# Kernel tuning notes

Measured on AMD Instinct MI355X. Metric: run time of the kernel, lower is better.

Reference implementation:

```python
import jax, jax.numpy as jnp
import numpy as np

# ---- config mirroring DetectionPostProcessV1 init + quant params ----
B, H, W, A, C = 8, 128, 128, 8, 8      # batch, feature HxW, anchors/cell, num_classes
STRIDE = 8
IMG_W, IMG_H = 1024, 1024               # image_size
INPUT_SHIFT = 4                          # kInputShift -> in_scale = 1/16
EXP_SHIFT = 4                            # from _gen_exp_table with in_scale 1/16
BOX_THR_INT = 9                          # ceil(0.55 * 2**INPUT_SHIFT)
NMS_THR = 128.0 / 256.0                  # ceil(0.5 * 2**kNmsThresholdShift) / 2**8
NMS_MARGIN = 0.0                         # nms_margin (quantized: ceil(0*16)/16)
PRE_K, POST_K = 1024, 300                # pre-NMS candidates, post_nms_top_k
CLASS_OFFSETS = jnp.zeros((C,), jnp.int32)
CLASS_SEP = 4096.0                       # coordinate offset for class-aware NMS


def setup_inputs() -> dict:
    key = jax.random.key(0)
    k1, _ = jax.random.split(key)
    # int8 repr of quantized head outputs (stored as int32 for jax indexing)
    data = jax.random.randint(k1, (B, A * (4 + C), H, W), -128, 128, dtype=jnp.int32)
    # grid anchors: 8 sizes per cell, stride-8 feature map
    sizes = np.array([16, 24, 32, 48, 64, 96, 128, 192], np.float32)
    ys = (np.arange(H, dtype=np.float32) + 0.5) * STRIDE
    xs = (np.arange(W, dtype=np.float32) + 0.5) * STRIDE
    cy, cx = np.meshgrid(ys, xs, indexing="ij")
    cx, cy = cx[..., None], cy[..., None]              # [H,W,1]
    w = np.broadcast_to(sizes, (H, W, A))
    h = np.broadcast_to(sizes, (H, W, A))
    anchors = np.stack([cx - w / 2, cy - h / 2, cx + w / 2, cy + h / 2], -1)
    anchors = jnp.asarray(anchors.reshape(-1, 4).astype(np.float32))  # [N,4] matches [H,W,A] flatten order
    # integer exp table, exactly as _gen_exp_table
    in_scale = 1.0 / (1 << INPUT_SHIFT)
    idx = np.arange(-128, 128, dtype=np.float32) * in_scale
    ev = np.exp(idx)
    exp_table = jnp.asarray(np.round(ev * (1 << EXP_SHIFT)).astype(np.int32))
    return {"data": data, "anchors": anchors, "exp_table": exp_table}


def _post_process(data, anchors, exp_table):
    N = H * W * A
    # [B, A*(4+C), H, W] -> [B, N, 4+C]
    x = data.reshape(B, A, 4 + C, H, W).transpose(0, 3, 4, 1, 2).reshape(B, N, 4 + C)
    box_d = x[..., :4]
    scores_i = x[..., 4:] + CLASS_OFFSETS                      # int scores with class offsets
    # decode: dx,dy via fixed-point shift; dw,dh via int exp table lookup
    dxy = box_d[..., :2].astype(jnp.float32) / (1 << INPUT_SHIFT)
    expv = exp_table[box_d[..., 2:4] + 128].astype(jnp.float32) / (1 << EXP_SHIFT)
    ctr = (anchors[:, :2] + anchors[:, 2:]) * 0.5              # [N,2]
    wh = anchors[:, 2:] - anchors[:, :2]
    pc = ctr + dxy * wh                                        # [B,N,2]
    pwh = wh * expv
    boxes = jnp.concatenate([pc - pwh * 0.5, pc + pwh * 0.5], -1)
    boxes = jnp.clip(boxes, 0.0, jnp.array([IMG_W, IMG_H, IMG_W, IMG_H], jnp.float32))
    # score filter
    best = scores_i.max(-1)
    label = scores_i.argmax(-1).astype(jnp.int32)
    valid = best >= BOX_THR_INT
    score = best.astype(jnp.float32) / (1 << INPUT_SHIFT)
    sc_masked = jnp.where(valid, score, -1e9)
    topv, topi = jax.lax.top_k(sc_masked, PRE_K)               # [B,PRE_K]
    bk = jnp.take_along_axis(boxes, topi[..., None], 1)        # [B,PRE_K,4]
    lk = jnp.take_along_axis(label, topi, 1)
    vk = topv > -1e8
    # class-aware NMS via coordinate offset trick
    ob = bk + lk[..., None].astype(jnp.float32) * CLASS_SEP
    area = (ob[..., 2] - ob[..., 0]) * (ob[..., 3] - ob[..., 1])
    lt = jnp.maximum(ob[:, :, None, :2], ob[:, None, :, :2])
    rb = jnp.minimum(ob[:, :, None, 2:], ob[:, None, :, 2:])
    whi = jnp.clip(rb - lt, 0.0)
    inter = whi[..., 0] * whi[..., 1]
    iou = inter / (area[:, :, None] + area[:, None, :] - inter + 1e-9)  # [B,PRE_K,PRE_K]
    idxr = jnp.arange(PRE_K)

    def body(i, sup):
        alive_i = ~jnp.take(sup, i, axis=1)                    # [B]
        iou_i = jnp.take(iou, i, axis=1)                       # [B,PRE_K]
        s_i = jnp.take(topv, i, axis=1)[:, None]
        cond = (alive_i[:, None] & (iou_i > NMS_THR)
                & (topv <= s_i - NMS_MARGIN) & (idxr > i)[None, :])
        return sup | cond

    sup = jax.lax.fori_loop(0, PRE_K, body, ~vk)
    keep = vk & ~sup
    fs = jnp.where(keep, topv, -1e9)
    outv, outi = jax.lax.top_k(fs, POST_K)
    boxes_out = jnp.take_along_axis(bk, outi[..., None], 1)
    labels = jnp.take_along_axis(lk, outi, 1)
    ok = outv > -1e8
    boxes_out = jnp.where(ok[..., None], boxes_out, 0.0)       # [B,POST_K,4]
    scores_out = jnp.where(ok, outv, 0.0)                      # [B,POST_K]
    labels_out = jnp.where(ok, labels, -1)                     # [B,POST_K]
    return boxes_out, scores_out, labels_out


def reference(data, anchors, exp_table):
    return _post_process(data, anchors, exp_table)
```

## Files before the change

### kernel.cpp

```cpp
#include <hip/hip_runtime.h>
#include <stdint.h>

#define Bb 8
#define PREK 1024
#define POSTK 300
#define NBIN 120
#define NCHUNK 512

__device__ __forceinline__ float clampb(float v){ return fminf(fmaxf(v, 0.0f), 1024.0f); }

__global__ void __launch_bounds__(256) k1_scores(const int* __restrict__ data,
                                                 unsigned short* __restrict__ sc16,
                                                 int* __restrict__ chist){
    int blk = blockIdx.x;
    int b = blk >> 7, h = blk & 127;
    int tid = threadIdx.x;
    int a = tid >> 5, wg = tid & 31;
    int w = wg << 2;
    const int* p = data + (((size_t)(b*96 + a*12 + 4)) << 14) + (h << 7) + w;
    int4 m = *(const int4*)p;
    int4 lb = make_int4(0,0,0,0);
#pragma unroll
    for (int c = 1; c < 8; ++c){
        int4 v = *(const int4*)(p + ((size_t)c << 14));
        if (v.x > m.x){ m.x = v.x; lb.x = c; }
        if (v.y > m.y){ m.y = v.y; lb.y = c; }
        if (v.z > m.z){ m.z = v.z; lb.z = c; }
        if (v.w > m.w){ m.w = v.w; lb.w = c; }
    }
    ushort4 st;
    st.x = (unsigned short)(((m.x + 128) << 8) | lb.x);
    st.y = (unsigned short)(((m.y + 128) << 8) | lb.y);
    st.z = (unsigned short)(((m.z + 128) << 8) | lb.z);
    st.w = (unsigned short)(((m.w + 128) << 8) | lb.w);
    *(ushort4*)(sc16 + (((size_t)(b*8 + a)) << 14) + (h << 7) + w) = st;

    __shared__ int hist[4][NBIN];
    for (int i = tid; i < 4*NBIN; i += 256) ((int*)hist)[i] = 0;
    __syncthreads();
    int q = wg >> 3;
    if (m.x >= 9) atomicAdd(&hist[q][m.x-9], 1);
    if (m.y >= 9) atomicAdd(&hist[q][m.y-9], 1);
    if (m.z >= 9) atomicAdd(&hist[q][m.z-9], 1);
    if (m.w >= 9) atomicAdd(&hist[q][m.w-9], 1);
    __syncthreads();
    int* cb = chist + ((size_t)(b*NCHUNK + h*4)) * NBIN;
    for (int i = tid; i < 4*NBIN; i += 256) cb[i] = ((int*)hist)[i];
}

__global__ void __launch_bounds__(256) k2_select(int* __restrict__ chist, int* __restrict__ gt,
                                                 int* __restrict__ Tb_, int* __restrict__ dmeta){
    int b = blockIdx.x, tid = threadIdx.x;
    __shared__ int hs2[2][NBIN];
    __shared__ int suf[128];
    __shared__ int Tsh;
    __shared__ int sb[512];
    if (tid == 0) Tsh = -1;
    int half = tid >> 7, bin = tid & 127;
    const int* cb = chist + (size_t)b * NCHUNK * NBIN;
    if (bin < NBIN){
        int s = 0;
        const int* p2 = cb + (size_t)half*256*NBIN + bin;
#pragma unroll 8
        for (int ch = 0; ch < 256; ++ch) s += p2[(size_t)ch * NBIN];
        hs2[half][bin] = s;
    }
    __syncthreads();
    int hbin = 0;
    if (tid < 128){
        hbin = (tid < NBIN) ? hs2[0][tid] + hs2[1][tid] : 0;
        suf[tid] = hbin;
    }
    __syncthreads();
    for (int off = 1; off < 128; off <<= 1){
        int v = 0;
        if (tid < 128 && tid + off < 128) v = suf[tid + off];
        __syncthreads();
        if (tid < 128) suf[tid] += v;
        __syncthreads();
    }
    if (tid < NBIN){
        gt[b*128 + tid] = suf[tid] - hbin;
        if (suf[tid] >= PREK) atomicMax(&Tsh, tid);
    }
    __syncthreads();
    int T = Tsh > 0 ? Tsh : 0;
    if (tid == 0) Tb_[b] = T;
    for (int k = tid; k < PREK; k += 256) dmeta[b*PREK + k] = -1;
    int i0 = tid, i1 = tid + 256;
    for (int abin = T; abin < NBIN; ++abin){
        int* basep = chist + (size_t)(b*NCHUNK) * NBIN + abin;
        int v0 = basep[(size_t)i0 * NBIN], v1 = basep[(size_t)i1 * NBIN];
        sb[i0] = v0; sb[i1] = v1;
        __syncthreads();
        for (int off = 1; off < 512; off <<= 1){
            int a0 = (i0 >= off) ? sb[i0 - off] : 0;
            int a1 = (i1 >= off) ? sb[i1 - off] : 0;
            __syncthreads();
            sb[i0] += a0; sb[i1] += a1;
            __syncthreads();
        }
        basep[(size_t)i0 * NBIN] = sb[i0] - v0;
        basep[(size_t)i1 * NBIN] = sb[i1] - v1;
        __syncthreads();
    }
}

__global__ void __launch_bounds__(256) k3_rank(const unsigned short* __restrict__ sc16,
                                               const int* __restrict__ chist,
                                               const int* __restrict__ gt, const int* __restrict__ Tb_,
                                               const int* __restrict__ data,
                                               const float* __restrict__ anchors,
                                               const int* __restrict__ etab,
                                               float4* __restrict__ dbox, int* __restrict__ dmeta){
    int blk = blockIdx.x;
    int b = blk >> 9, ci = blk & 511;
    int tid = threadIdx.x;
    int h = ci >> 2, w0 = (ci & 3) << 5;
    __shared__ unsigned short sc[256];
    __shared__ int wcnt[4][NBIN];
    if (tid < 64){
        int a = tid & 7, wq = tid >> 3;
        ushort4 v4 = *(const ushort4*)(sc16 + (((size_t)(b*8 + a)) << 14) + (h << 7) + w0 + (wq << 2));
        sc[(wq*4 + 0)*8 + a] = v4.x;
        sc[(wq*4 + 1)*8 + a] = v4.y;
        sc[(wq*4 + 2)*8 + a] = v4.z;
        sc[(wq*4 + 3)*8 + a] = v4.w;
    }
    for (int i = tid; i < 4*NBIN; i += 256) ((int*)wcnt)[i] = 0;
    int T = Tb_[b];
    __syncthreads();
    unsigned short v = sc[tid];
    int s = (int)(v >> 8) - 128;
    int bin = s - 9;
    bool qual = (bin >= T);
    int wv = tid >> 6, lane = tid & 63;
    if (qual) atomicAdd(&wcnt[wv][bin], 1);
    __syncthreads();
    int myeq = 0;
    {
        unsigned long long low = (1ull << lane) - 1ull;
        for (int vb = T; vb < NBIN; ++vb){
            unsigned long long bal = __ballot(qual && bin == vb);
            if (!bal) continue;
            if (qual && bin == vb) myeq = __popcll(bal & low);
        }
    }
    if (!qual) return;
    int cross = 0;
    for (int w2 = 0; w2 < wv; ++w2) cross += wcnt[w2][bin];
    int rank = gt[b*128 + bin] + chist[((size_t)(b*NCHUNK) + ci)*NBIN + bin] + cross + myeq;
    if (rank < PREK){
        int n = ci*256 + tid;
        int a = n & 7, wc = (n >> 3) & 127;
        const int* p = data + (((size_t)(b*96 + a*12)) << 14) + (h << 7) + wc;
        int d0 = p[0], d1 = p[1 << 14], d2 = p[2 << 14], d3 = p[3 << 14];
        float4 an = ((const float4*)anchors)[n];
        float cx = __fmul_rn(__fadd_rn(an.x, an.z), 0.5f);
        float cy = __fmul_rn(__fadd_rn(an.y, an.w), 0.5f);
        float wx = __fsub_rn(an.z, an.x), wy = __fsub_rn(an.w, an.y);
        float dx = __fmul_rn((float)d0, 0.0625f), dy = __fmul_rn((float)d1, 0.0625f);
        float ex = __fmul_rn((float)etab[d2 + 128], 0.0625f);
        float ey = __fmul_rn((float)etab[d3 + 128], 0.0625f);
        float pcx = __fadd_rn(cx, __fmul_rn(dx, wx));
        float pcy = __fadd_rn(cy, __fmul_rn(dy, wy));
        float hx = __fmul_rn(__fmul_rn(wx, ex), 0.5f);
        float hy = __fmul_rn(__fmul_rn(wy, ey), 0.5f);
        float x1 = clampb(__fsub_rn(pcx, hx)), y1 = clampb(__fsub_rn(pcy, hy));
        float x2 = clampb(__fadd_rn(pcx, hx)), y2 = clampb(__fadd_rn(pcy, hy));
        dbox[b*PREK + rank] = make_float4(x1, y1, x2, y2);
        dmeta[b*PREK + rank] = (int)v;
    }
}

__global__ void __launch_bounds__(512, 2) k45_nms_out(const float4* __restrict__ dbox,
                                                      const int* __restrict__ dmeta,
                                                      float* __restrict__ out){
    int b = blockIdx.x, tid = threadIdx.x, lane = tid & 63, wv = tid >> 6;
    __shared__ float X1[1024], Y1[1024], X2[1024], Y2[1024], AR[1024];
    __shared__ unsigned char KEEP[1024];
    __shared__ int wq[8][8], wq2[8][8];
    __shared__ int cbs[8], ccn[8];
    __shared__ int wcn[8];
    __shared__ int pbase;

    int v0 = dmeta[b*PREK + tid];
    int v1 = dmeta[b*PREK + 512 + tid];
    float4 bb0 = dbox[b*PREK + tid];
    float4 bb1 = dbox[b*PREK + 512 + tid];
    bool valid0 = (v0 >= 0), valid1 = (v1 >= 0);
    int lc0 = valid0 ? (v0 & 255) : -1;
    int lc1 = valid1 ? (v1 & 255) : -1;
    KEEP[tid] = 0; KEEP[tid + 512] = 0;
    if (tid == 0) pbase = 0;
    int win0 = 0, win1 = 0;
#pragma unroll
    for (int c = 0; c < 8; ++c){
        unsigned long long bal0 = __ballot(lc0 == c);
        unsigned long long bal1 = __ballot(lc1 == c);
        if (lane == 0){ wq[wv][c] = __popcll(bal0); wq2[wv][c] = __popcll(bal1); }
        if (lc0 == c) win0 = __popcll(bal0 & ((1ull << lane) - 1ull));
        if (lc1 == c) win1 = __popcll(bal1 & ((1ull << lane) - 1ull));
    }
    __syncthreads();
    if (tid < 8){
        int run = 0;
        for (int w2 = 0; w2 < 8; ++w2){ int t = wq[w2][tid];  wq[w2][tid]  = run; run += t; }
        for (int w2 = 0; w2 < 8; ++w2){ int t = wq2[w2][tid]; wq2[w2][tid] = run; run += t; }
        ccn[tid] = run;
    }
    __syncthreads();
    if (tid == 0){
        int run = 0;
        for (int c = 0; c < 8; ++c){ cbs[c] = run; run += ccn[c]; }
    }
    __syncthreads();
    int p0 = 0, p1 = 0;
    if (valid0){
        p0 = cbs[lc0] + wq[wv][lc0] + win0;
        float off = (float)(lc0 << 12);
        float ox1 = __fadd_rn(bb0.x, off), oy1 = __fadd_rn(bb0.y, off);
        float ox2 = __fadd_rn(bb0.z, off), oy2 = __fadd_rn(bb0.w, off);
        X1[p0] = ox1; Y1[p0] = oy1; X2[p0] = ox2; Y2[p0] = oy2;
        AR[p0] = __fmul_rn(__fsub_rn(ox2, ox1), __fsub_rn(oy2, oy1));
    }
    if (valid1){
        p1 = cbs[lc1] + wq2[wv][lc1] + win1;
        float off = (float)(lc1 << 12);
        float ox1 = __fadd_rn(bb1.x, off), oy1 = __fadd_rn(bb1.y, off);
        float ox2 = __fadd_rn(bb1.z, off), oy2 = __fadd_rn(bb1.w, off);
        X1[p1] = ox1; Y1[p1] = oy1; X2[p1] = ox2; Y2[p1] = oy2;
        AR[p1] = __fmul_rn(__fsub_rn(ox2, ox1), __fsub_rn(oy2, oy1));
    }
    __syncthreads();

    {
        int M = ccn[wv], base = cbs[wv];
        if (M > 0 && M <= 256){
            float rx1[4], ry1[4], rx2[4], ry2[4], rar[4];
#pragma unroll
            for (int g = 0; g < 4; ++g){
                int r = g*64 + lane;
                int ad = base + ((r < M) ? r : 0);
                rx1[g]=X1[ad]; ry1[g]=Y1[ad]; rx2[g]=X2[ad]; ry2[g]=Y2[ad]; rar[g]=AR[ad];
            }
            unsigned long long mk[4][4];
#pragma unroll
            for (int g = 0; g < 4; ++g)
#pragma unroll
                for (int w2 = 0; w2 < 4; ++w2) mk[g][w2] = 0ull;

#pragma unroll
            for (int jw = 0; jw < 4; ++jw){
                if (jw*64 < M){
                    int limj = M - jw*64; if (limj > 64) limj = 64;
#pragma unroll 8
                    for (int jl = 0; jl < 64; ++jl){
                        if (jl < limj){
                            int j = jw*64 + jl;
                            float jx1 = __shfl(rx1[jw], jl);
                            float jy1 = __shfl(ry1[jw], jl);
                            float jx2 = __shfl(rx2[jw], jl);
                            float jy2 = __shfl(ry2[jw], jl);
                            float jar = __shfl(rar[jw], jl);
#pragma unroll
                            for (int g = 0; g < 4; ++g){
                                if (g*64 < M){
                                    int i = g*64 + lane;
                                    float wx = fmaxf(__fsub_rn(fminf(rx2[g], jx2), fmaxf(rx1[g], jx1)), 0.0f);
                                    float wy = fmaxf(__fsub_rn(fminf(ry2[g], jy2), fmaxf(ry1[g], jy1)), 0.0f);
                                    float inter = __fmul_rn(wx, wy);
                                    float den = __fadd_rn(__fsub_rn(__fadd_rn(rar[g], jar), inter), 1e-9f);
                                    bool o = (__fdiv_rn(inter, den) > 0.5f) && (j > i);
                                    mk[g][jw] |= o ? (1ull << jl) : 0ull;
                                }
                            }
                        }
                    }
                }
            }

            unsigned long long r0=0ull, r1=0ull, r2=0ull, r3=0ull;
#pragma unroll
            for (int iw = 0; iw < 4; ++iw){
                if (iw*64 < M){
                    int limi = M - iw*64; if (limi > 64) limi = 64;
#pragma unroll 8
                    for (int il = 0; il < 64; ++il){
                        if (il < limi){
                            unsigned long long cur = (iw==0)?r0:(iw==1)?r1:(iw==2)?r2:r3;
                            unsigned long long w0 = __shfl(mk[iw][0], il);
                            unsigned long long w1 = __shfl(mk[iw][1], il);
                            unsigned long long w2_ = __shfl(mk[iw][2], il);
                            unsigned long long w3_ = __shfl(mk[iw][3], il);
                            unsigned long long msk = ((cur >> il) & 1ull) ? 0ull : ~0ull;
                            r0 |= w0 & msk; r1 |= w1 & msk; r2 |= w2_ & msk; r3 |= w3_ & msk;
                        }
                    }
                }
            }
#pragma unroll
            for (int g = 0; g < 4; ++g){
                int r = g*64 + lane;
                unsigned long long rg = (g==0)?r0:(g==1)?r1:(g==2)?r2:r3;
                if (r < M) KEEP[base + r] = (unsigned char)(((rg >> lane) & 1ull) ^ 1ull);
            }
        } else if (M > 256){
            for (int m = lane; m < M; m += 64) KEEP[base+m] = 0;
            for (int i = 0; i < M; ++i){
                if (KEEP[base+i]) continue;
                float xi1 = X1[base+i], yi1 = Y1[base+i];
                float xi2 = X2[base+i], yi2 = Y2[base+i], ai = AR[base+i];
                for (int j = i + 1 + lane; j < M; j += 64){
                    if (KEEP[base+j]) continue;
                    float wx = fmaxf(__fsub_rn(fminf(xi2, X2[base+j]), fmaxf(xi1, X1[base+j])), 0.0f);
                    float wy = fmaxf(__fsub_rn(fminf(yi2, Y2[base+j]), fmaxf(yi1, Y1[base+j])), 0.0f);
                    float inter = __fmul_rn(wx, wy);
                    float den = __fadd_rn(__fsub_rn(__fadd_rn(ai, AR[base+j]), inter), 1e-9f);
                    if (__fdiv_rn(inter, den) > 0.5f) KEEP[base+j] = 1;
                }
            }
            for (int m = lane; m < M; m += 64) KEEP[base+m] ^= 1;
        }
    }
    __syncthreads();

    float* boxes  = out;
    float* scores = out + Bb*POSTK*4;
    float* labs   = out + Bb*POSTK*5;
#pragma unroll
    for (int pass = 0; pass < 2; ++pass){
        bool vld   = pass ? valid1 : valid0;
        int  pp    = pass ? p1 : p0;
        int  lcc   = pass ? lc1 : lc0;
        int  vv    = pass ? v1 : v0;
        float4 bbb = pass ? bb1 : bb0;
        bool kp = vld && (KEEP[pp] != 0);
        unsigned long long bal = __ballot(kp);
        if (lane == 0) wcn[wv] = __popcll(bal);
        __syncthreads();
        if (tid == 0){
            int r = pbase;
            for (int w2 = 0; w2 < 8; ++w2){ int t = wcn[w2]; wcn[w2] = r; r += t; }
            pbase = r;
        }
        __syncthreads();
        int pos = wcn[wv] + __popcll(bal & ((1ull << lane) - 1ull));
        if (kp && pos < POSTK){
            float sval = __fmul_rn((float)((vv >> 8) - 128), 0.0625f);
            int o = (b*POSTK + pos)*4;
            boxes[o+0] = bbb.x; boxes[o+1] = bbb.y; boxes[o+2] = bbb.z; boxes[o+3] = bbb.w;
            scores[b*POSTK + pos] = sval;
            labs[b*POSTK + pos] = (float)lcc;
        }
        __syncthreads();
    }
    int tot = pbase < POSTK ? pbase : POSTK;
    if (tid >= tot && tid < POSTK){
        int o = (b*POSTK + tid)*4;
        boxes[o+0] = 0.f; boxes[o+1] = 0.f; boxes[o+2] = 0.f; boxes[o+3] = 0.f;
        scores[b*POSTK + tid] = 0.f;
        labs[b*POSTK + tid] = -1.0f;
    }
}

extern "C" void kernel_launch(void* const* d_in, const int* in_sizes, int n_in,
                              void* d_out, int out_size, void* d_ws, size_t ws_size,
                              hipStream_t stream) {
    const int*   data    = (const int*)d_in[0];
    const float* anchors = (const float*)d_in[1];
    const int*   etab    = (const int*)d_in[2];
    float* out = (float*)d_out;

    char* ws = (char*)d_ws;
    size_t off = 0;
    auto alloc = [&](size_t bytes)->char*{ char* p = ws + off; off += (bytes + 255) & ~(size_t)255; return p; };
    unsigned short* sc16 = (unsigned short*)alloc((size_t)Bb*8*16384*2);
    int* chist           = (int*)alloc((size_t)Bb*NCHUNK*NBIN*4);
    int* gt              = (int*)alloc((size_t)Bb*128*4);
    int* Tb_             = (int*)alloc((size_t)Bb*4);
    float4* dbox         = (float4*)alloc((size_t)Bb*PREK*16);
    int* dmeta           = (int*)alloc((size_t)Bb*PREK*4);
    (void)ws_size; (void)in_sizes; (void)n_in; (void)out_size;

    k1_scores<<<Bb*128, 256, 0, stream>>>(data, sc16, chist);
    k2_select<<<Bb, 256, 0, stream>>>(chist, gt, Tb_, dmeta);
    k3_rank<<<Bb*NCHUNK, 256, 0, stream>>>(sc16, chist, gt, Tb_, data, anchors, etab, dbox, dmeta);
    k45_nms_out<<<Bb, 512, 0, stream>>>(dbox, dmeta, out);
}
```

Measured before the change: 156.2 us.

## Specialize NMS bitmask path by class size and widen histogram reduction

After: 143.9 us. 7.9% less time.

```diff
diff --git a/kernel.cpp b/kernel.cpp
--- a/kernel.cpp
+++ b/kernel.cpp
@@ -48,27 +48,35 @@
     for (int i = tid; i < 4*NBIN; i += 256) cb[i] = ((int*)hist)[i];
 }
 
-__global__ void __launch_bounds__(256) k2_select(int* __restrict__ chist, int* __restrict__ gt,
-                                                 int* __restrict__ Tb_, int* __restrict__ dmeta){
+__global__ void __launch_bounds__(1024) k2_select(int* __restrict__ chist, int* __restrict__ gt,
+                                                  int* __restrict__ Tb_, int* __restrict__ dmeta){
     int b = blockIdx.x, tid = threadIdx.x;
-    __shared__ int hs2[2][NBIN];
+    __shared__ int part[8][NBIN];
+    __shared__ int hs[NBIN];
     __shared__ int suf[128];
     __shared__ int Tsh;
     __shared__ int sb[512];
     if (tid == 0) Tsh = -1;
-    int half = tid >> 7, bin = tid & 127;
     const int* cb = chist + (size_t)b * NCHUNK * NBIN;
-    if (bin < NBIN){
+    if (tid < 8*NBIN){
+        int g = tid / NBIN, bin = tid - g*NBIN;
         int s = 0;
-        const int* p2 = cb + (size_t)half*256*NBIN + bin;
+        const int* p2 = cb + (size_t)g*64*NBIN + bin;
 #pragma unroll 8
-        for (int ch = 0; ch < 256; ++ch) s += p2[(size_t)ch * NBIN];
-        hs2[half][bin] = s;
+        for (int ch = 0; ch < 64; ++ch) s += p2[(size_t)ch * NBIN];
+        part[g][bin] = s;
+    }
+    __syncthreads();
+    if (tid < NBIN){
+        int s = 0;
+#pragma unroll
+        for (int g = 0; g < 8; ++g) s += part[g][tid];
+        hs[tid] = s;
     }
     __syncthreads();
     int hbin = 0;
     if (tid < 128){
-        hbin = (tid < NBIN) ? hs2[0][tid] + hs2[1][tid] : 0;
+        hbin = (tid < NBIN) ? hs[tid] : 0;
         suf[tid] = hbin;
     }
     __syncthreads();
@@ -86,22 +94,20 @@
     __syncthreads();
     int T = Tsh > 0 ? Tsh : 0;
     if (tid == 0) Tb_[b] = T;
-    for (int k = tid; k < PREK; k += 256) dmeta[b*PREK + k] = -1;
-    int i0 = tid, i1 = tid + 256;
+    dmeta[b*PREK + tid] = -1;
     for (int abin = T; abin < NBIN; ++abin){
         int* basep = chist + (size_t)(b*NCHUNK) * NBIN + abin;
-        int v0 = basep[(size_t)i0 * NBIN], v1 = basep[(size_t)i1 * NBIN];
-        sb[i0] = v0; sb[i1] = v1;
+        int v = 0;
+        if (tid < 512){ v = basep[(size_t)tid * NBIN]; sb[tid] = v; }
         __syncthreads();
         for (int off = 1; off < 512; off <<= 1){
-            int a0 = (i0 >= off) ? sb[i0 - off] : 0;
-            int a1 = (i1 >= off) ? sb[i1 - off] : 0;
+            int a2 = 0;
+            if (tid < 512 && tid >= off) a2 = sb[tid - off];
             __syncthreads();
-            sb[i0] += a0; sb[i1] += a1;
+            if (tid < 512) sb[tid] += a2;
             __syncthreads();
         }
-        basep[(size_t)i0 * NBIN] = sb[i0] - v0;
-        basep[(size_t)i1 * NBIN] = sb[i1] - v1;
+        if (tid < 512) basep[(size_t)tid * NBIN] = sb[tid] - v;
         __syncthreads();
     }
 }
@@ -173,7 +179,81 @@
     }
 }
 
-__global__ void __launch_bounds__(512, 2) k45_nms_out(const float4* __restrict__ dbox,
+template<int NG>
+__device__ __forceinline__ void nms_reg(const float* __restrict__ X1, const float* __restrict__ Y1,
+                                        const float* __restrict__ X2, const float* __restrict__ Y2,
+                                        const float* __restrict__ AR,
+                                        int base, int M, int lane, unsigned char* __restrict__ KEEP){
+    float rx1[NG], ry1[NG], rx2[NG], ry2[NG], rar[NG];
+#pragma unroll
+    for (int g = 0; g < NG; ++g){
+        int r = g*64 + lane;
+        int ad = base + ((r < M) ? r : 0);
+        rx1[g]=X1[ad]; ry1[g]=Y1[ad]; rx2[g]=X2[ad]; ry2[g]=Y2[ad]; rar[g]=AR[ad];
+    }
+    unsigned long long mk[NG][NG];
+#pragma unroll
+    for (int g = 0; g < NG; ++g)
+#pragma unroll
+        for (int c = 0; c < NG; ++c) mk[g][c] = 0ull;
+
+#pragma unroll
+    for (int jw = 0; jw < NG; ++jw){
+        if (jw*64 < M){
+            int limj = M - jw*64; if (limj > 64) limj = 64;
+#pragma unroll 4
+            for (int jl = 0; jl < 64; ++jl){
+                if (jl < limj){
+                    float jx1 = __shfl(rx1[jw], jl);
+                    float jy1 = __shfl(ry1[jw], jl);
+                    float jx2 = __shfl(rx2[jw], jl);
+                    float jy2 = __shfl(ry2[jw], jl);
+                    float jar = __fmul_rn(__fsub_rn(jx2, jx1), __fsub_rn(jy2, jy1));
+#pragma unroll
+                    for (int g = 0; g < NG; ++g){
+                        if (g > jw) continue;
+                        bool jgi = (g < jw) ? true : (lane < jl);
+                        float wx = fmaxf(__fsub_rn(fminf(rx2[g], jx2), fmaxf(rx1[g], jx1)), 0.0f);
+                        float wy = fmaxf(__fsub_rn(fminf(ry2[g], jy2), fmaxf(ry1[g], jy1)), 0.0f);
+                        float inter = __fmul_rn(wx, wy);
+                        float den = __fadd_rn(__fsub_rn(__fadd_rn(rar[g], jar), inter), 1e-9f);
+                        bool o = (__fdiv_rn(inter, den) > 0.5f) && jgi;
+                        mk[g][jw] |= o ? (1ull << jl) : 0ull;
+                    }
+                }
+            }
+        }
+    }
+
+    unsigned long long rem[NG];
+#pragma unroll
+    for (int g = 0; g < NG; ++g) rem[g] = 0ull;
+#pragma unroll
+    for (int iw = 0; iw < NG; ++iw){
+        if (iw*64 < M){
+            int limi = M - iw*64; if (limi > 64) limi = 64;
+#pragma unroll 4
+            for (int il = 0; il < 64; ++il){
+                if (il < limi){
+                    unsigned long long msk = ((rem[iw] >> il) & 1ull) ? 0ull : ~0ull;
+#pragma unroll
+                    for (int w = iw; w < NG; ++w){
+                        unsigned long long rw = __shfl(mk[iw][w], il);
+                        rem[w] |= rw & msk;
+                    }
+                }
+            }
+        }
+    }
+#pragma unroll
+    for (int g = 0; g < NG; ++g){
+        int r = g*64 + lane;
+        unsigned long long rg = rem[g];
+        if (r < M) KEEP[base + r] = (unsigned char)(((rg >> lane) & 1ull) ^ 1ull);
+    }
+}
+
+__global__ void __launch_bounds__(512, 1) k45_nms_out(const float4* __restrict__ dbox,
                                                       const int* __restrict__ dmeta,
                                                       float* __restrict__ out){
     int b = blockIdx.x, tid = threadIdx.x, lane = tid & 63, wv = tid >> 6;
@@ -236,91 +316,27 @@
 
     {
         int M = ccn[wv], base = cbs[wv];
-        if (M > 0 && M <= 256){
-            float rx1[4], ry1[4], rx2[4], ry2[4], rar[4];
-#pragma unroll
-            for (int g = 0; g < 4; ++g){
-                int r = g*64 + lane;
-                int ad = base + ((r < M) ? r : 0);
-                rx1[g]=X1[ad]; ry1[g]=Y1[ad]; rx2[g]=X2[ad]; ry2[g]=Y2[ad]; rar[g]=AR[ad];
-            }
-            unsigned long long mk[4][4];
-#pragma unroll
-            for (int g = 0; g < 4; ++g)
-#pragma unroll
-                for (int w2 = 0; w2 < 4; ++w2) mk[g][w2] = 0ull;
-
-#pragma unroll
-            for (int jw = 0; jw < 4; ++jw){
-                if (jw*64 < M){
-                    int limj = M - jw*64; if (limj > 64) limj = 64;
-#pragma unroll 8
-                    for (int jl = 0; jl < 64; ++jl){
-                        if (jl < limj){
-                            int j = jw*64 + jl;
-                            float jx1 = __shfl(rx1[jw], jl);
-                            float jy1 = __shfl(ry1[jw], jl);
-                            float jx2 = __shfl(rx2[jw], jl);
-                            float jy2 = __shfl(ry2[jw], jl);
-                            float jar = __shfl(rar[jw], jl);
-#pragma unroll
-                            for (int g = 0; g < 4; ++g){
-                                if (g*64 < M){
-                                    int i = g*64 + lane;
-                                    float wx = fmaxf(__fsub_rn(fminf(rx2[g], jx2), fmaxf(rx1[g], jx1)), 0.0f);
-                                    float wy = fmaxf(__fsub_rn(fminf(ry2[g], jy2), fmaxf(ry1[g], jy1)), 0.0f);
-                                    float inter = __fmul_rn(wx, wy);
-                                    float den = __fadd_rn(__fsub_rn(__fadd_rn(rar[g], jar), inter), 1e-9f);
-                                    bool o = (__fdiv_rn(inter, den) > 0.5f) && (j > i);
-                                    mk[g][jw] |= o ? (1ull << jl) : 0ull;
-                                }
-                            }
-                        }
+        if (M > 0){
+            if (M <= 128)      nms_reg<2>(X1, Y1, X2, Y2, AR, base, M, lane, KEEP);
+            else if (M <= 192) nms_reg<3>(X1, Y1, X2, Y2, AR, base, M, lane, KEEP);
+            else if (M <= 256) nms_reg<4>(X1, Y1, X2, Y2, AR, base, M, lane, KEEP);
+            else {
+                for (int m = lane; m < M; m += 64) KEEP[base+m] = 0;
+                for (int i = 0; i < M; ++i){
+                    if (KEEP[base+i]) continue;
+                    float xi1 = X1[base+i], yi1 = Y1[base+i];
+                    float xi2 = X2[base+i], yi2 = Y2[base+i], ai = AR[base+i];
+                    for (int j = i + 1 + lane; j < M; j += 64){
+                        if (KEEP[base+j]) continue;
+                        float wx = fmaxf(__fsub_rn(fminf(xi2, X2[base+j]), fmaxf(xi1, X1[base+j])), 0.0f);
+                        float wy = fmaxf(__fsub_rn(fminf(yi2, Y2[base+j]), fmaxf(yi1, Y1[base+j])), 0.0f);
+                        float inter = __fmul_rn(wx, wy);
+                        float den = __fadd_rn(__fsub_rn(__fadd_rn(ai, AR[base+j]), inter), 1e-9f);
+                        if (__fdiv_rn(inter, den) > 0.5f) KEEP[base+j] = 1;
                     }
                 }
+                for (int m = lane; m < M; m += 64) KEEP[base+m] ^= 1;
             }
-
-            unsigned long long r0=0ull, r1=0ull, r2=0ull, r3=0ull;
-#pragma unroll
-            for (int iw = 0; iw < 4; ++iw){
-                if (iw*64 < M){
-                    int limi = M - iw*64; if (limi > 64) limi = 64;
-#pragma unroll 8
-                    for (int il = 0; il < 64; ++il){
-                        if (il < limi){
-                            unsigned long long cur = (iw==0)?r0:(iw==1)?r1:(iw==2)?r2:r3;
-                            unsigned long long w0 = __shfl(mk[iw][0], il);
-                            unsigned long long w1 = __shfl(mk[iw][1], il);
-                            unsigned long long w2_ = __shfl(mk[iw][2], il);
-                            unsigned long long w3_ = __shfl(mk[iw][3], il);
-                            unsigned long long msk = ((cur >> il) & 1ull) ? 0ull : ~0ull;
-                            r0 |= w0 & msk; r1 |= w1 & msk; r2 |= w2_ & msk; r3 |= w3_ & msk;
-                        }
-                    }
-                }
-            }
-#pragma unroll
-            for (int g = 0; g < 4; ++g){
-                int r = g*64 + lane;
-                unsigned long long rg = (g==0)?r0:(g==1)?r1:(g==2)?r2:r3;
-                if (r < M) KEEP[base + r] = (unsigned char)(((rg >> lane) & 1ull) ^ 1ull);
-            }
-        } else if (M > 256){
-            for (int m = lane; m < M; m += 64) KEEP[base+m] = 0;
-            for (int i = 0; i < M; ++i){
-                if (KEEP[base+i]) continue;
-                float xi1 = X1[base+i], yi1 = Y1[base+i];
-                float xi2 = X2[base+i], yi2 = Y2[base+i], ai = AR[base+i];
-                for (int j = i + 1 + lane; j < M; j += 64){
-                    if (KEEP[base+j]) continue;
-                    float wx = fmaxf(__fsub_rn(fminf(xi2, X2[base+j]), fmaxf(xi1, X1[base+j])), 0.0f);
-                    float wy = fmaxf(__fsub_rn(fminf(yi2, Y2[base+j]), fmaxf(yi1, Y1[base+j])), 0.0f);
-                    float inter = __fmul_rn(wx, wy);
-                    float den = __fadd_rn(__fsub_rn(__fadd_rn(ai, AR[base+j]), inter), 1e-9f);
-                    if (__fdiv_rn(inter, den) > 0.5f) KEEP[base+j] = 1;
-                }
-            }
-            for (int m = lane; m < M; m += 64) KEEP[base+m] ^= 1;
         }
     }
     __syncthreads();
@@ -384,7 +400,7 @@
     (void)ws_size; (void)in_sizes; (void)n_in; (void)out_size;
 
     k1_scores<<<Bb*128, 256, 0, stream>>>(data, sc16, chist);
-    k2_select<<<Bb, 256, 0, stream>>>(chist, gt, Tb_, dmeta);
+    k2_select<<<Bb, 1024, 0, stream>>>(chist, gt, Tb_, dmeta);
     k3_rank<<<Bb*NCHUNK, 256, 0, stream>>>(sc16, chist, gt, Tb_, data, anchors, etab, dbox, dmeta);
     k45_nms_out<<<Bb, 512, 0, stream>>>(dbox, dmeta, out);
 }
```
